# Kernel optimization log

Hardware: AMD Instinct MI355X
Metric: run time of the kernel (lower is better)

The kernel has to match this reference:

```python
import jax, jax.numpy as jnp
import numpy as np


def setup_inputs() -> dict:
    key = jax.random.key(0)
    k1, k2 = jax.random.split(key)
    B, C, H, W_ = 16, 512, 64, 64
    x = jax.random.normal(k1, (B, C, H, W_), dtype=jnp.float32)
    W = jax.random.normal(k2, (C, C), dtype=jnp.float32) * (1.0 / np.sqrt(C))
    return {"x": x, "W": W}


def reference(x, W):
    B, C, H, Wd = x.shape
    hw = H * Wd
    x1 = x.reshape(B, C, hw)                      # [B, C, HW]
    # linearW applied to x1^T: [B, HW, C] @ W^T -> [B, HW, C]
    x1_corr = jnp.einsum('bch,dc->bhd', x1, W)    # [B, HW, C]
    s = jnp.einsum('bch,bhd->bcd', x1, x1_corr)   # [B, C, C]
    a = jax.nn.softmax(s, axis=2)
    a = jax.nn.softmax(a, axis=1)
    out = jnp.einsum('bcd,bdh->bch', a, x1) + x1  # [B, C, HW]
    return out.reshape(B, C, H, Wd)
```

## Files before the change

### kernel.cpp

```cpp
#include <hip/hip_runtime.h>


typedef __attribute__((ext_vector_type(8))) short bf16x8;
typedef __attribute__((ext_vector_type(4))) float f32x4;

#define DEVINL __device__ __forceinline__
#define CFENCE() asm volatile("" ::: "memory")

DEVINL unsigned short f2bf(float f) {
  union { float f; unsigned int u; } c; c.f = f;
  unsigned int u = c.u;
  u += 0x7fffu + ((u >> 16) & 1u);
  return (unsigned short)(u >> 16);
}

DEVINL float bf2f(unsigned short h) {
  union { unsigned int u; float f; } c; c.u = ((unsigned int)h) << 16;
  return c.f;
}

DEVINL void gld_lds16(const unsigned short* g, unsigned short* l) {
  __builtin_amdgcn_global_load_lds(
      (const __attribute__((address_space(1))) unsigned int*)g,
      (__attribute__((address_space(3))) unsigned int*)l,
      16 , 0, 0);
}

template<int N> DEVINL void vm_wait() {
  if constexpr (N == 0)       asm volatile("s_waitcnt vmcnt(0)" ::: "memory");
  else if constexpr (N == 2)  asm volatile("s_waitcnt vmcnt(2)" ::: "memory");
  else if constexpr (N == 4)  asm volatile("s_waitcnt vmcnt(4)" ::: "memory");
  else if constexpr (N == 8)  asm volatile("s_waitcnt vmcnt(8)" ::: "memory");
  else static_assert(N < 0, "unsupported vmcnt");
}

DEVINL void sym_tile_decode(int t, int& tm, int& tn) {
  if (t < 4)      { tm = 0; tn = t; }
  else if (t < 7) { tm = 1; tn = t - 3; }
  else if (t < 9) { tm = 2; tn = t - 5; }
  else            { tm = 3; tn = 3; }
}

__global__ __launch_bounds__(256)
void cvt_kernel(const float* __restrict__ in, unsigned short* __restrict__ out, int n4) {
  int i = blockIdx.x * 256 + threadIdx.x;
  const int stride = gridDim.x * 256;
  for (; i < n4; i += stride) {
    float4 v = ((const float4*)in)[i];
    unsigned int lo = (unsigned int)f2bf(v.x) | ((unsigned int)f2bf(v.y) << 16);
    unsigned int hi = (unsigned int)f2bf(v.z) | ((unsigned int)f2bf(v.w) << 16);
    uint2 o; o.x = lo; o.y = hi;
    ((uint2*)out)[i] = o;
  }
}

__global__ __launch_bounds__(256)
void fused_cvt_transpose(const float* __restrict__ x, unsigned short* __restrict__ x_bf,
                         unsigned short* __restrict__ xT) {
  __shared__ unsigned int T[2][32][68];
  const int tid = threadIdx.x;
  const int b  = blockIdx.y;
  const int hs = blockIdx.x & 31;
  const int ct = blockIdx.x >> 5;
  const int h0 = hs * 128;
  const int hq = tid & 7;
  const int c2 = tid >> 3;

  uint4 pa[2], pb[2];
  long long rowA[2];
  #pragma unroll
  for (int hh = 0; hh < 2; ++hh) {
    const int hcol = h0 + hh * 64 + hq * 8;
    rowA[hh] = (long long)(b * 512 + ct * 64 + 2 * c2) * 4096 + hcol;
    float4 a0 = *(const float4*)(x + rowA[hh]);
    float4 a1 = *(const float4*)(x + rowA[hh] + 4);
    float4 b0 = *(const float4*)(x + rowA[hh] + 4096);
    float4 b1 = *(const float4*)(x + rowA[hh] + 4100);
    unsigned short ha[8], hb[8];
    ha[0]=f2bf(a0.x); ha[1]=f2bf(a0.y); ha[2]=f2bf(a0.z); ha[3]=f2bf(a0.w);
    ha[4]=f2bf(a1.x); ha[5]=f2bf(a1.y); ha[6]=f2bf(a1.z); ha[7]=f2bf(a1.w);
    hb[0]=f2bf(b0.x); hb[1]=f2bf(b0.y); hb[2]=f2bf(b0.z); hb[3]=f2bf(b0.w);
    hb[4]=f2bf(b1.x); hb[5]=f2bf(b1.y); hb[6]=f2bf(b1.z); hb[7]=f2bf(b1.w);
    pa[hh].x = (unsigned int)ha[0] | ((unsigned int)ha[1] << 16);
    pa[hh].y = (unsigned int)ha[2] | ((unsigned int)ha[3] << 16);
    pa[hh].z = (unsigned int)ha[4] | ((unsigned int)ha[5] << 16);
    pa[hh].w = (unsigned int)ha[6] | ((unsigned int)ha[7] << 16);
    pb[hh].x = (unsigned int)hb[0] | ((unsigned int)hb[1] << 16);
    pb[hh].y = (unsigned int)hb[2] | ((unsigned int)hb[3] << 16);
    pb[hh].z = (unsigned int)hb[4] | ((unsigned int)hb[5] << 16);
    pb[hh].w = (unsigned int)hb[6] | ((unsigned int)hb[7] << 16);
    uint4 u0, u1;
    u0.x = (unsigned int)ha[0] | ((unsigned int)hb[0] << 16);
    u0.y = (unsigned int)ha[1] | ((unsigned int)hb[1] << 16);
    u0.z = (unsigned int)ha[2] | ((unsigned int)hb[2] << 16);
    u0.w = (unsigned int)ha[3] | ((unsigned int)hb[3] << 16);
    u1.x = (unsigned int)ha[4] | ((unsigned int)hb[4] << 16);
    u1.y = (unsigned int)ha[5] | ((unsigned int)hb[5] << 16);
    u1.z = (unsigned int)ha[6] | ((unsigned int)hb[6] << 16);
    u1.w = (unsigned int)ha[7] | ((unsigned int)hb[7] << 16);
    *(uint4*)&T[hh][c2][hq * 8]     = u0;
    *(uint4*)&T[hh][c2][hq * 8 + 4] = u1;
  }
  asm volatile("s_waitcnt lgkmcnt(0)" ::: "memory");
  __builtin_amdgcn_s_barrier();
  #pragma unroll
  for (int hh = 0; hh < 2; ++hh) {
    *(uint4*)(x_bf + rowA[hh])        = pa[hh];
    *(uint4*)(x_bf + rowA[hh] + 4096) = pb[hh];
  }
  const int h = tid >> 2, seg = tid & 3;
  #pragma unroll
  for (int hh = 0; hh < 2; ++hh) {
    unsigned int uu[8];
    #pragma unroll
    for (int i = 0; i < 8; ++i) uu[i] = T[hh][seg * 8 + i][h];
    unsigned int* dst = (unsigned int*)(xT +
        ((long long)(b * 4096 + h0 + hh * 64 + h) * 512 + ct * 64 + seg * 16));
    uint4 o0, o1;
    o0.x = uu[0]; o0.y = uu[1]; o0.z = uu[2]; o0.w = uu[3];
    o1.x = uu[4]; o1.y = uu[5]; o1.z = uu[6]; o1.w = uu[7];
    *(uint4*)dst = o0;
    *((uint4*)dst + 1) = o1;
  }
}

__global__ __launch_bounds__(256)
void gemm_gsym(const unsigned short* __restrict__ X, float* __restrict__ P) {
  constexpr int HALF = 128 * 32;
  __shared__ unsigned short As[3 * HALF];
  __shared__ unsigned short Bs[3 * HALF];
  const int tid = threadIdx.x;
  const int l   = tid & 63;
  const int w   = tid >> 6;
  const int wr  = w >> 1, wc = w & 1;
  const int b   = blockIdx.y;
  const int t   = blockIdx.x >> 2;
  const int split = blockIdx.x & 3;
  int tm, tn; sym_tile_decode(t, tm, tn);

  const unsigned short* Ab = X + (long long)b * 2097152 + (long long)(tm * 128) * 4096;
  const unsigned short* Bb = X + (long long)b * 2097152 + (long long)(tn * 128) * 4096;

  f32x4 acc[4][4];
  #pragma unroll
  for (int m = 0; m < 4; ++m)
    #pragma unroll
    for (int n = 0; n < 4; ++n) acc[m][n] = (f32x4){0.f, 0.f, 0.f, 0.f};

  const int srow = tid >> 2;
  const int scol = ((tid & 3) ^ ((tid >> 3) & 3)) * 8;
  const int ch8  = (((l >> 4) ^ ((l >> 1) & 3)) * 8);

  auto stage = [&](int buf, int k0) {
    #pragma unroll
    for (int i = 0; i < 2; ++i)
      gld_lds16(Ab + (long long)(i * 64 + srow) * 4096 + k0 + scol, &As[buf * HALF + i * 2048 + tid * 8]);
    #pragma unroll
    for (int i = 0; i < 2; ++i)
      gld_lds16(Bb + (long long)(i * 64 + srow) * 4096 + k0 + scol, &Bs[buf * HALF + i * 2048 + tid * 8]);
  };
  auto compute = [&](int buf) {
    bf16x8 af[4], bfr[4];
    #pragma unroll
    for (int m = 0; m < 4; ++m)
      af[m] = *(const bf16x8*)&As[buf * HALF + (wr * 64 + m * 16 + (l & 15)) * 32 + ch8];
    #pragma unroll
    for (int n = 0; n < 4; ++n)
      bfr[n] = *(const bf16x8*)&Bs[buf * HALF + (wc * 64 + n * 16 + (l & 15)) * 32 + ch8];
    __builtin_amdgcn_s_setprio(1);
    #pragma unroll
    for (int m = 0; m < 4; ++m)
      #pragma unroll
      for (int n = 0; n < 4; ++n)
        acc[m][n] = __builtin_amdgcn_mfma_f32_16x16x32_bf16(af[m], bfr[n], acc[m][n], 0, 0, 0);
    __builtin_amdgcn_s_setprio(0);
  };

  const int k_beg = split * 1024;
  constexpr int NK = 32;
  stage(0, k_beg);
  stage(1, k_beg + 32);
  int cb = 0, sbuf = 2, ks = k_beg + 64;
  for (int k = 0; k < NK - 2; ++k) {
    stage(sbuf, ks);
    ks += 32;
    sbuf = (sbuf == 2) ? 0 : sbuf + 1;
    vm_wait<8>();
    CFENCE(); __builtin_amdgcn_s_barrier(); CFENCE();
    compute(cb);
    CFENCE(); __builtin_amdgcn_s_barrier(); CFENCE();
    cb = (cb == 2) ? 0 : cb + 1;
  }
  vm_wait<4>();
  CFENCE(); __builtin_amdgcn_s_barrier(); CFENCE();
  compute(cb);
  cb = (cb == 2) ? 0 : cb + 1;
  vm_wait<0>();
  CFENCE(); __builtin_amdgcn_s_barrier(); CFENCE();
  compute(cb);

  float* Pt = P + (((long long)b * 10 + t) * 4 + split) * 16384;
  const int cc = l & 15, r4 = (l >> 4) * 4;
  #pragma unroll
  for (int m = 0; m < 4; ++m) {
    #pragma unroll
    for (int n = 0; n < 4; ++n) {
      const int row = wr * 64 + m * 16 + r4;
      const int col = wc * 64 + n * 16 + cc;
      #pragma unroll
      for (int j = 0; j < 4; ++j)
        Pt[(row + j) * 128 + col] = acc[m][n][j];
    }
  }
}

__global__ __launch_bounds__(256)
void reduce_mirror(const float* __restrict__ P, unsigned short* __restrict__ G) {
  __shared__ unsigned short T[128 * 129];
  const int tid = threadIdx.x;
  const int b = blockIdx.y;
  const int t = blockIdx.x;
  int tm, tn; sym_tile_decode(t, tm, tn);
  const float* Pt = P + ((long long)(b * 10 + t) * 4) * 16384;
  unsigned short* Gb = G + (long long)b * 262144;

  #pragma unroll
  for (int e = 0; e < 16; ++e) {
    const int v = e * 256 + tid;
    float4 s0 = ((const float4*)Pt)[v];
    float4 s1 = ((const float4*)(Pt + 16384))[v];
    float4 s2 = ((const float4*)(Pt + 32768))[v];
    float4 s3 = ((const float4*)(Pt + 49152))[v];
    unsigned int h0 = f2bf(s0.x + s1.x + s2.x + s3.x);
    unsigned int h1 = f2bf(s0.y + s1.y + s2.y + s3.y);
    unsigned int h2 = f2bf(s0.z + s1.z + s2.z + s3.z);
    unsigned int h3 = f2bf(s0.w + s1.w + s2.w + s3.w);
    const int idx = v * 4;
    const int r = idx >> 7, c = idx & 127;
    unsigned int* gp = (unsigned int*)(Gb + (long long)(tm * 128 + r) * 512 + tn * 128 + c);
    gp[0] = h0 | (h1 << 16);
    gp[1] = h2 | (h3 << 16);
    unsigned short* tp = &T[r * 129 + c];
    tp[0] = (unsigned short)h0; tp[1] = (unsigned short)h1;
    tp[2] = (unsigned short)h2; tp[3] = (unsigned short)h3;
  }
  if (tm != tn) {
    __syncthreads();
    #pragma unroll
    for (int e = 0; e < 16; ++e) {
      const int idx = (e * 256 + tid) * 4;
      const int r = idx >> 7, c = idx & 127;
      unsigned int o0 = T[(c + 0) * 129 + r], o1 = T[(c + 1) * 129 + r];
      unsigned int o2 = T[(c + 2) * 129 + r], o3 = T[(c + 3) * 129 + r];
      unsigned int* gp = (unsigned int*)(Gb + (long long)(tn * 128 + r) * 512 + tm * 128 + c);
      gp[0] = o0 | (o1 << 16);
      gp[1] = o2 | (o3 << 16);
    }
  }
}

template<int FR>
__global__ __launch_bounds__(256)
void gemm_bt4(const unsigned short* __restrict__ A, const unsigned short* __restrict__ B,
              float* __restrict__ C,
              int N, int K, int sA, int sB,
              long long bsA, long long bsB, long long bsC, int Ntiles) {
  constexpr int BMN = FR * 32;
  constexpr int ISS = BMN / 64;
  constexpr int HALF = BMN * 32;
  constexpr int NLOAD = 2 * ISS;
  __shared__ unsigned short As[3 * HALF];
  __shared__ unsigned short Bs[3 * HALF];

  const int tid = threadIdx.x;
  const int l   = tid & 63;
  const int w   = tid >> 6;
  const int wr  = w >> 1, wc = w & 1;
  const int bz  = blockIdx.y;
  const int tm  = blockIdx.x / Ntiles;
  const int tn  = blockIdx.x % Ntiles;

  const unsigned short* Ab = A + bz * bsA + (long long)(tm * BMN) * sA;
  const unsigned short* Bb = B + bz * bsB + (long long)(tn * BMN) * sB;

  f32x4 acc[FR][FR];
  #pragma unroll
  for (int m = 0; m < FR; ++m)
    #pragma unroll
    for (int n = 0; n < FR; ++n) acc[m][n] = (f32x4){0.f, 0.f, 0.f, 0.f};

  const int srow = tid >> 2;
  const int scol = ((tid & 3) ^ ((tid >> 3) & 3)) * 8;
  const int ch8  = (((l >> 4) ^ ((l >> 1) & 3)) * 8);

  auto stage = [&](int buf, int k0) {
    #pragma unroll
    for (int i = 0; i < ISS; ++i)
      gld_lds16(Ab + (long long)(i * 64 + srow) * sA + k0 + scol, &As[buf * HALF + i * 2048 + tid * 8]);
    #pragma unroll
    for (int i = 0; i < ISS; ++i)
      gld_lds16(Bb + (long long)(i * 64 + srow) * sB + k0 + scol, &Bs[buf * HALF + i * 2048 + tid * 8]);
  };
  auto compute = [&](int buf) {
    bf16x8 af[FR], bfr[FR];
    #pragma unroll
    for (int m = 0; m < FR; ++m)
      af[m] = *(const bf16x8*)&As[buf * HALF + (wr * (FR * 16) + m * 16 + (l & 15)) * 32 + ch8];
    #pragma unroll
    for (int n = 0; n < FR; ++n)
      bfr[n] = *(const bf16x8*)&Bs[buf * HALF + (wc * (FR * 16) + n * 16 + (l & 15)) * 32 + ch8];
    __builtin_amdgcn_s_setprio(1);
    #pragma unroll
    for (int m = 0; m < FR; ++m)
      #pragma unroll
      for (int n = 0; n < FR; ++n)
        acc[m][n] = __builtin_amdgcn_mfma_f32_16x16x32_bf16(af[m], bfr[n], acc[m][n], 0, 0, 0);
    __builtin_amdgcn_s_setprio(0);
  };

  const int nk = K >> 5;
  stage(0, 0);
  stage(1, 32);
  int cb = 0, sbuf = 2, ks = 64;
  for (int k = 0; k < nk - 2; ++k) {
    stage(sbuf, ks);
    ks += 32;
    sbuf = (sbuf == 2) ? 0 : sbuf + 1;
    vm_wait<2 * NLOAD>();
    CFENCE(); __builtin_amdgcn_s_barrier(); CFENCE();
    compute(cb);
    CFENCE(); __builtin_amdgcn_s_barrier(); CFENCE();
    cb = (cb == 2) ? 0 : cb + 1;
  }
  vm_wait<NLOAD>();
  CFENCE(); __builtin_amdgcn_s_barrier(); CFENCE();
  compute(cb);
  cb = (cb == 2) ? 0 : cb + 1;
  vm_wait<0>();
  CFENCE(); __builtin_amdgcn_s_barrier(); CFENCE();
  compute(cb);

  const int cc = l & 15, r4 = (l >> 4) * 4;
  const int row0 = tm * BMN + wr * (FR * 16);
  const int col0 = tn * BMN + wc * (FR * 16);
  #pragma unroll
  for (int m = 0; m < FR; ++m) {
    #pragma unroll
    for (int n = 0; n < FR; ++n) {
      const int row = row0 + m * 16 + r4;
      const int col = col0 + n * 16 + cc;
      long long base = bz * bsC + (long long)row * N + col;
      #pragma unroll
      for (int j = 0; j < 4; ++j)
        C[base + (long long)j * N] = acc[m][n][j];
    }
  }
}

__global__ __launch_bounds__(256)
void row_softmax_kernel(const float* __restrict__ s, unsigned short* __restrict__ p_bf) {
  __shared__ float red[4], red2[4];
  const float* p = s + (long long)blockIdx.x * 512;
  unsigned short* q = p_bf + (long long)blockIdx.x * 512;
  const int tid = threadIdx.x;
  float v0 = p[tid], v1 = p[tid + 256];
  float m = fmaxf(v0, v1);
  #pragma unroll
  for (int i = 1; i < 64; i <<= 1) m = fmaxf(m, __shfl_xor(m, i));
  if ((tid & 63) == 0) red[tid >> 6] = m;
  __syncthreads();
  m = fmaxf(fmaxf(red[0], red[1]), fmaxf(red[2], red[3]));
  float e0 = __expf(v0 - m), e1 = __expf(v1 - m);
  float sum = e0 + e1;
  #pragma unroll
  for (int i = 1; i < 64; i <<= 1) sum += __shfl_xor(sum, i);
  if ((tid & 63) == 0) red2[tid >> 6] = sum;
  __syncthreads();
  sum = (red2[0] + red2[1]) + (red2[2] + red2[3]);
  float inv = 1.0f / sum;
  q[tid] = f2bf(e0 * inv);
  q[tid + 256] = f2bf(e1 * inv);
}

__global__ __launch_bounds__(256)
void col_softmax_kernel(const unsigned short* __restrict__ p_bf, unsigned short* __restrict__ a_bf) {
  __shared__ float cs[8][32];
  const int tid = threadIdx.x;
  const int dl = tid & 31;
  const int st = tid >> 5;
  const int d  = blockIdx.x * 32 + dl;
  const long long base = (long long)blockIdx.y * 262144 + d;
  const unsigned short* p = p_bf + base;
  float sum = 0.f;
  #pragma unroll 4
  for (int c = st * 64; c < st * 64 + 64; ++c)
    sum += __expf(bf2f(p[(long long)c * 512]));
  cs[st][dl] = sum;
  __syncthreads();
  if (st == 0) {
    float s = ((cs[0][dl] + cs[1][dl]) + (cs[2][dl] + cs[3][dl]))
            + ((cs[4][dl] + cs[5][dl]) + (cs[6][dl] + cs[7][dl]));
    cs[0][dl] = 1.0f / s;
  }
  __syncthreads();
  const float inv = cs[0][dl];
  unsigned short* q = a_bf + base;
  #pragma unroll 4
  for (int c = st * 64; c < st * 64 + 64; ++c) {
    float v = __expf(bf2f(p[(long long)c * 512])) * inv;
    if (c == d) v += 1.0f;
    q[(long long)c * 512] = f2bf(v);
  }
}

extern "C" void kernel_launch(void* const* d_in, const int* in_sizes, int n_in,
                              void* d_out, int out_size, void* d_ws, size_t ws_size,
                              hipStream_t stream) {
  (void)in_sizes; (void)n_in; (void)out_size; (void)ws_size;
  const float* x = (const float*)d_in[0];
  const float* W = (const float*)d_in[1];
  float* out = (float*)d_out;
  char* ws = (char*)d_ws;

  unsigned short* x_bf = (unsigned short*)d_out;
  float* P = (float*)((char*)d_out + 67108864);
  unsigned short* p_bf = (unsigned short*)((char*)d_out + 67108864);

  unsigned short* xT   = (unsigned short*)ws;
  unsigned short* G_bf = (unsigned short*)(ws + 67108864);
  float*          s_f  = (float*)(ws + 75497472);
  unsigned short* W_bf = (unsigned short*)(ws + 92274688);
  unsigned short* a_bf = G_bf;

  fused_cvt_transpose<<<dim3(256, 16), 256, 0, stream>>>(x, x_bf, xT);
  cvt_kernel<<<256, 256, 0, stream>>>(W, W_bf, 65536);

  gemm_gsym<<<dim3(40, 16), 256, 0, stream>>>(x_bf, P);

  reduce_mirror<<<dim3(10, 16), 256, 0, stream>>>(P, G_bf);

  gemm_bt4<2><<<dim3(64, 16), 256, 0, stream>>>(
      G_bf, W_bf, s_f,
      512, 512, 512, 512, 262144LL, 0LL, 262144LL, 8);

  row_softmax_kernel<<<8192, 256, 0, stream>>>(s_f, p_bf);
  col_softmax_kernel<<<dim3(16, 16), 256, 0, stream>>>(p_bf, a_bf);

  gemm_bt4<4><<<dim3(128, 16), 256, 0, stream>>>(
      a_bf, xT, out,
      4096, 512, 512, 512, 262144LL, 2097152LL, 2097152LL, 32);
}
```

Baseline: 186.5 us.

## Specialize GEMMs with constant shapes and enlarge output GEMM tile to 128x256

Replaces the templated gemm_bt4 with two shape-specialized kernels. gemm_s hardcodes strides and loop counts for the 64x64 score GEMM. gemm_out uses a 128x256 tile in which each wave owns a 64-column strip across all 128 rows, so more MFMAs run per LDS load and the grid halves. The trade-off is higher accumulator register pressure (32 f32x4 per lane), which lowers occupancy, plus more LDS per block.

```diff
diff --git a/kernel.cpp b/kernel.cpp
--- a/kernel.cpp
+++ b/kernel.cpp
@@ -30,7 +30,9 @@
   if constexpr (N == 0)       asm volatile("s_waitcnt vmcnt(0)" ::: "memory");
   else if constexpr (N == 2)  asm volatile("s_waitcnt vmcnt(2)" ::: "memory");
   else if constexpr (N == 4)  asm volatile("s_waitcnt vmcnt(4)" ::: "memory");
+  else if constexpr (N == 6)  asm volatile("s_waitcnt vmcnt(6)" ::: "memory");
   else if constexpr (N == 8)  asm volatile("s_waitcnt vmcnt(8)" ::: "memory");
+  else if constexpr (N == 12) asm volatile("s_waitcnt vmcnt(12)" ::: "memory");
   else static_assert(N < 0, "unsupported vmcnt");
 }
 
@@ -259,16 +261,10 @@
   }
 }
 
-template<int FR>
-__global__ __launch_bounds__(256)
-void gemm_bt4(const unsigned short* __restrict__ A, const unsigned short* __restrict__ B,
-              float* __restrict__ C,
-              int N, int K, int sA, int sB,
-              long long bsA, long long bsB, long long bsC, int Ntiles) {
-  constexpr int BMN = FR * 32;
-  constexpr int ISS = BMN / 64;
-  constexpr int HALF = BMN * 32;
-  constexpr int NLOAD = 2 * ISS;
+__global__ __launch_bounds__(256)
+void gemm_s(const unsigned short* __restrict__ A, const unsigned short* __restrict__ B,
+            float* __restrict__ C) {
+  constexpr int HALF = 64 * 32;
   __shared__ unsigned short As[3 * HALF];
   __shared__ unsigned short Bs[3 * HALF];
 
@@ -277,62 +273,57 @@
   const int w   = tid >> 6;
   const int wr  = w >> 1, wc = w & 1;
   const int bz  = blockIdx.y;
-  const int tm  = blockIdx.x / Ntiles;
-  const int tn  = blockIdx.x % Ntiles;
-
-  const unsigned short* Ab = A + bz * bsA + (long long)(tm * BMN) * sA;
-  const unsigned short* Bb = B + bz * bsB + (long long)(tn * BMN) * sB;
-
-  f32x4 acc[FR][FR];
-  #pragma unroll
-  for (int m = 0; m < FR; ++m)
-    #pragma unroll
-    for (int n = 0; n < FR; ++n) acc[m][n] = (f32x4){0.f, 0.f, 0.f, 0.f};
+  const int tm  = blockIdx.x >> 3;
+  const int tn  = blockIdx.x & 7;
+
+  const unsigned short* Ab = A + (long long)bz * 262144 + (long long)(tm * 64) * 512;
+  const unsigned short* Bb = B + (long long)(tn * 64) * 512;
+
+  f32x4 acc[2][2];
+  #pragma unroll
+  for (int m = 0; m < 2; ++m)
+    #pragma unroll
+    for (int n = 0; n < 2; ++n) acc[m][n] = (f32x4){0.f, 0.f, 0.f, 0.f};
 
   const int srow = tid >> 2;
   const int scol = ((tid & 3) ^ ((tid >> 3) & 3)) * 8;
   const int ch8  = (((l >> 4) ^ ((l >> 1) & 3)) * 8);
 
   auto stage = [&](int buf, int k0) {
-    #pragma unroll
-    for (int i = 0; i < ISS; ++i)
-      gld_lds16(Ab + (long long)(i * 64 + srow) * sA + k0 + scol, &As[buf * HALF + i * 2048 + tid * 8]);
-    #pragma unroll
-    for (int i = 0; i < ISS; ++i)
-      gld_lds16(Bb + (long long)(i * 64 + srow) * sB + k0 + scol, &Bs[buf * HALF + i * 2048 + tid * 8]);
+    gld_lds16(Ab + (long long)srow * 512 + k0 + scol, &As[buf * HALF + tid * 8]);
+    gld_lds16(Bb + (long long)srow * 512 + k0 + scol, &Bs[buf * HALF + tid * 8]);
   };
   auto compute = [&](int buf) {
-    bf16x8 af[FR], bfr[FR];
-    #pragma unroll
-    for (int m = 0; m < FR; ++m)
-      af[m] = *(const bf16x8*)&As[buf * HALF + (wr * (FR * 16) + m * 16 + (l & 15)) * 32 + ch8];
-    #pragma unroll
-    for (int n = 0; n < FR; ++n)
-      bfr[n] = *(const bf16x8*)&Bs[buf * HALF + (wc * (FR * 16) + n * 16 + (l & 15)) * 32 + ch8];
+    bf16x8 af[2], bfr[2];
+    #pragma unroll
+    for (int m = 0; m < 2; ++m)
+      af[m] = *(const bf16x8*)&As[buf * HALF + (wr * 32 + m * 16 + (l & 15)) * 32 + ch8];
+    #pragma unroll
+    for (int n = 0; n < 2; ++n)
+      bfr[n] = *(const bf16x8*)&Bs[buf * HALF + (wc * 32 + n * 16 + (l & 15)) * 32 + ch8];
     __builtin_amdgcn_s_setprio(1);
     #pragma unroll
-    for (int m = 0; m < FR; ++m)
+    for (int m = 0; m < 2; ++m)
       #pragma unroll
-      for (int n = 0; n < FR; ++n)
+      for (int n = 0; n < 2; ++n)
         acc[m][n] = __builtin_amdgcn_mfma_f32_16x16x32_bf16(af[m], bfr[n], acc[m][n], 0, 0, 0);
     __builtin_amdgcn_s_setprio(0);
   };
 
-  const int nk = K >> 5;
   stage(0, 0);
   stage(1, 32);
   int cb = 0, sbuf = 2, ks = 64;
-  for (int k = 0; k < nk - 2; ++k) {
+  for (int k = 0; k < 14; ++k) {
     stage(sbuf, ks);
     ks += 32;
     sbuf = (sbuf == 2) ? 0 : sbuf + 1;
-    vm_wait<2 * NLOAD>();
+    vm_wait<4>();
     CFENCE(); __builtin_amdgcn_s_barrier(); CFENCE();
     compute(cb);
     CFENCE(); __builtin_amdgcn_s_barrier(); CFENCE();
     cb = (cb == 2) ? 0 : cb + 1;
   }
-  vm_wait<NLOAD>();
+  vm_wait<2>();
   CFENCE(); __builtin_amdgcn_s_barrier(); CFENCE();
   compute(cb);
   cb = (cb == 2) ? 0 : cb + 1;
@@ -341,18 +332,109 @@
   compute(cb);
 
   const int cc = l & 15, r4 = (l >> 4) * 4;
-  const int row0 = tm * BMN + wr * (FR * 16);
-  const int col0 = tn * BMN + wc * (FR * 16);
-  #pragma unroll
-  for (int m = 0; m < FR; ++m) {
-    #pragma unroll
-    for (int n = 0; n < FR; ++n) {
+  const int row0 = tm * 64 + wr * 32;
+  const int col0 = tn * 64 + wc * 32;
+  #pragma unroll
+  for (int m = 0; m < 2; ++m) {
+    #pragma unroll
+    for (int n = 0; n < 2; ++n) {
       const int row = row0 + m * 16 + r4;
       const int col = col0 + n * 16 + cc;
-      long long base = bz * bsC + (long long)row * N + col;
+      long long base = (long long)bz * 262144 + (long long)row * 512 + col;
       #pragma unroll
       for (int j = 0; j < 4; ++j)
-        C[base + (long long)j * N] = acc[m][n][j];
+        C[base + (long long)j * 512] = acc[m][n][j];
+    }
+  }
+}
+
+__global__ __launch_bounds__(256)
+void gemm_out(const unsigned short* __restrict__ A, const unsigned short* __restrict__ B,
+              float* __restrict__ C) {
+  constexpr int HALF_A = 128 * 32;
+  constexpr int HALF_B = 256 * 32;
+  __shared__ unsigned short As[3 * HALF_A];
+  __shared__ unsigned short Bs[3 * HALF_B];
+
+  const int tid = threadIdx.x;
+  const int l   = tid & 63;
+  const int w   = tid >> 6;
+  const int bz  = blockIdx.y;
+  const int tm  = blockIdx.x >> 4;
+  const int tn  = blockIdx.x & 15;
+
+  const unsigned short* Ab = A + (long long)bz * 262144  + (long long)(tm * 128) * 512;
+  const unsigned short* Bb = B + (long long)bz * 2097152 + (long long)(tn * 256) * 512;
+
+  f32x4 acc[8][4];
+  #pragma unroll
+  for (int m = 0; m < 8; ++m)
+    #pragma unroll
+    for (int n = 0; n < 4; ++n) acc[m][n] = (f32x4){0.f, 0.f, 0.f, 0.f};
+
+  const int srow = tid >> 2;
+  const int scol = ((tid & 3) ^ ((tid >> 3) & 3)) * 8;
+  const int ch8  = (((l >> 4) ^ ((l >> 1) & 3)) * 8);
+
+  auto stage = [&](int buf, int k0) {
+    #pragma unroll
+    for (int i = 0; i < 2; ++i)
+      gld_lds16(Ab + (long long)(i * 64 + srow) * 512 + k0 + scol, &As[buf * HALF_A + i * 2048 + tid * 8]);
+    #pragma unroll
+    for (int i = 0; i < 4; ++i)
+      gld_lds16(Bb + (long long)(i * 64 + srow) * 512 + k0 + scol, &Bs[buf * HALF_B + i * 2048 + tid * 8]);
+  };
+  auto compute = [&](int buf) {
+    bf16x8 af[8], bfr[4];
+    #pragma unroll
+    for (int m = 0; m < 8; ++m)
+      af[m] = *(const bf16x8*)&As[buf * HALF_A + (m * 16 + (l & 15)) * 32 + ch8];
+    #pragma unroll
+    for (int n = 0; n < 4; ++n)
+      bfr[n] = *(const bf16x8*)&Bs[buf * HALF_B + (w * 64 + n * 16 + (l & 15)) * 32 + ch8];
+    __builtin_amdgcn_s_setprio(1);
+    #pragma unroll
+    for (int m = 0; m < 8; ++m)
+      #pragma unroll
+      for (int n = 0; n < 4; ++n)
+        acc[m][n] = __builtin_amdgcn_mfma_f32_16x16x32_bf16(af[m], bfr[n], acc[m][n], 0, 0, 0);
+    __builtin_amdgcn_s_setprio(0);
+  };
+
+  stage(0, 0);
+  stage(1, 32);
+  int cb = 0, sbuf = 2, ks = 64;
+  for (int k = 0; k < 14; ++k) {
+    stage(sbuf, ks);
+    ks += 32;
+    sbuf = (sbuf == 2) ? 0 : sbuf + 1;
+    vm_wait<12>();
+    CFENCE(); __builtin_amdgcn_s_barrier(); CFENCE();
+    compute(cb);
+    CFENCE(); __builtin_amdgcn_s_barrier(); CFENCE();
+    cb = (cb == 2) ? 0 : cb + 1;
+  }
+  vm_wait<6>();
+  CFENCE(); __builtin_amdgcn_s_barrier(); CFENCE();
+  compute(cb);
+  cb = (cb == 2) ? 0 : cb + 1;
+  vm_wait<0>();
+  CFENCE(); __builtin_amdgcn_s_barrier(); CFENCE();
+  compute(cb);
+
+  const int cc = l & 15, r4 = (l >> 4) * 4;
+  const int row0 = tm * 128;
+  const int col0 = tn * 256 + w * 64;
+  #pragma unroll
+  for (int m = 0; m < 8; ++m) {
+    #pragma unroll
+    for (int n = 0; n < 4; ++n) {
+      const int row = row0 + m * 16 + r4;
+      const int col = col0 + n * 16 + cc;
+      long long base = (long long)bz * 2097152 + (long long)row * 4096 + col;
+      #pragma unroll
+      for (int j = 0; j < 4; ++j)
+        C[base + (long long)j * 4096] = acc[m][n][j];
     }
   }
 }
@@ -439,14 +521,10 @@
 
   reduce_mirror<<<dim3(10, 16), 256, 0, stream>>>(P, G_bf);
 
-  gemm_bt4<2><<<dim3(64, 16), 256, 0, stream>>>(
-      G_bf, W_bf, s_f,
-      512, 512, 512, 512, 262144LL, 0LL, 262144LL, 8);
+  gemm_s<<<dim3(64, 16), 256, 0, stream>>>(G_bf, W_bf, s_f);
 
   row_softmax_kernel<<<8192, 256, 0, stream>>>(s_f, p_bf);
   col_softmax_kernel<<<dim3(16, 16), 256, 0, stream>>>(p_bf, a_bf);
 
-  gemm_bt4<4><<<dim3(128, 16), 256, 0, stream>>>(
-      a_bf, xT, out,
-      4096, 512, 512, 512, 262144LL, 2097152LL, 2097152LL, 32);
-}
+  gemm_out<<<dim3(64, 16), 256, 0, stream>>>(a_bf, xT, out);
+}
```

Result: no change. 189.0 us (+1.3%).
